# Optimization experiments

Hardware: AMD Instinct MI355X
Metric: run time of the kernel (lower is better)

The kernel has to match this reference:

```python
import jax, jax.numpy as jnp
from jax import lax
import numpy as np

B, T, D_IN, H, L, D_OUT = 1024, 512, 6, 128, 3, 1


def _lstm_layer(xs, w_ih, w_hh, b_ih, b_hh):
    """xs: [B, T, Din]; w_ih: [4H, Din]; w_hh: [4H, H]. PyTorch gate order i,f,g,o."""
    Bq = xs.shape[0]
    Hq = w_hh.shape[1]
    # Precompute the input projection for all timesteps (compute-dense part).
    x_proj = jnp.einsum('btd,gd->btg', xs, w_ih) + (b_ih + b_hh)  # [B, T, 4H]

    def step(carry, xp):
        h, c = carry
        gates = xp + h @ w_hh.T  # [B, 4H]
        i, f, g, o = jnp.split(gates, 4, axis=-1)
        i = jax.nn.sigmoid(i)
        f = jax.nn.sigmoid(f)
        g = jnp.tanh(g)
        o = jax.nn.sigmoid(o)
        c = f * c + i * g
        h = o * jnp.tanh(c)
        return (h, c), h

    h0 = jnp.zeros((Bq, Hq), xs.dtype)
    c0 = jnp.zeros((Bq, Hq), xs.dtype)
    (_, _), hs = lax.scan(step, (h0, c0), jnp.swapaxes(x_proj, 0, 1))  # hs: [T, B, H]
    return jnp.swapaxes(hs, 0, 1)  # [B, T, H]


def setup_inputs() -> dict:
    key = jax.random.key(0)
    ks = jax.random.split(key, 16)
    s = 1.0 / np.sqrt(H)  # PyTorch LSTM init scale
    inp = {"x": jax.random.normal(ks[0], (B, T, D_IN), dtype=jnp.float32)}
    din = D_IN
    for l in range(L):
        inp[f"w_ih{l}"] = jax.random.uniform(ks[1 + 4 * l], (4 * H, din), minval=-s, maxval=s, dtype=jnp.float32)
        inp[f"w_hh{l}"] = jax.random.uniform(ks[2 + 4 * l], (4 * H, H), minval=-s, maxval=s, dtype=jnp.float32)
        inp[f"b_ih{l}"] = jax.random.uniform(ks[3 + 4 * l], (4 * H,), minval=-s, maxval=s, dtype=jnp.float32)
        inp[f"b_hh{l}"] = jax.random.uniform(ks[4 + 4 * l], (4 * H,), minval=-s, maxval=s, dtype=jnp.float32)
        din = H
    inp["fc_w"] = jax.random.uniform(ks[13], (D_OUT, H), minval=-s, maxval=s, dtype=jnp.float32)
    inp["fc_b"] = jax.random.uniform(ks[14], (D_OUT,), minval=-s, maxval=s, dtype=jnp.float32)
    return inp


def reference(x, w_ih0, w_hh0, b_ih0, b_hh0, w_ih1, w_hh1, b_ih1, b_hh1,
              w_ih2, w_hh2, b_ih2, b_hh2, fc_w, fc_b):
    # 3-layer LSTM (inference: dropout between layers is identity) + final Linear on last timestep.
    h = _lstm_layer(x, w_ih0, w_hh0, b_ih0, b_hh0)
    h = _lstm_layer(h, w_ih1, w_hh1, b_ih1, b_hh1)
    h = _lstm_layer(h, w_ih2, w_hh2, b_ih2, b_hh2)
    return h[:, -1, :] @ fc_w.T + fc_b  # [B, 1]
```

## Files before the change

### kernel.cpp

```cpp
#include <hip/hip_runtime.h>

#define TLEN  512
#define HID   128
#define RSLOT 16
#define QD    4

typedef __attribute__((ext_vector_type(8))) short          bf16x8;
typedef __attribute__((ext_vector_type(4))) float          f32x4;
typedef __attribute__((ext_vector_type(4))) unsigned short u16x4;
typedef unsigned long long u64;

#define LOG2E  1.4426950408889634f
#define LOG2E2 2.8853900817779268f

__device__ __forceinline__ unsigned short f2bf(float f) {
    union { float f; unsigned u; } v; v.f = f;
    unsigned r = v.u + 0x7fffu + ((v.u >> 16) & 1u);
    return (unsigned short)(r >> 16);
}
__device__ __forceinline__ unsigned short f2bf_fast(float f) {
    union { float f; unsigned u; } v; v.f = f;
    return (unsigned short)((v.u + 0x8000u) >> 16);
}

__device__ __forceinline__ float sig_ps(float xs) {
    return __builtin_amdgcn_rcpf(1.0f + __builtin_exp2f(-xs));
}
__device__ __forceinline__ float tanh_ps(float xs) {
    return 2.0f * __builtin_amdgcn_rcpf(1.0f + __builtin_exp2f(-xs)) - 1.0f;
}

__device__ __forceinline__ int flag_peek(const int* f) {
    return __hip_atomic_load(f, __ATOMIC_RELAXED, __HIP_MEMORY_SCOPE_AGENT);
}
__device__ __forceinline__ int flag_spin(const int* f, int v) {
    int x = flag_peek(f);
    while (x < v) { __builtin_amdgcn_s_sleep(1); x = flag_peek(f); }
    return x;
}
__device__ __forceinline__ void flag_pub(int* f, int v) {
    __hip_atomic_store(f, v, __ATOMIC_RELAXED, __HIP_MEMORY_SCOPE_WORKGROUP);
}

template<int MODE, bool CONS, bool PROD, bool WFC>
__device__ __forceinline__ void run_layer_p(
    const float* __restrict__ xin,
    const u64* __restrict__ rin, u64* __restrict__ rout,
    const int* pin_flag, int* cout_flag, const int* cin_flag, int* pout_flag,
    const float* __restrict__ wih, const float* __restrict__ whh,
    const float* __restrict__ bih, const float* __restrict__ bhh,
    unsigned short (* __restrict__ Abuf)[8 * 512],
    float* __restrict__ fcred,
    const int tid, const int wave, const int lane,
    const int n16, const int quad, const int bbase)
{
    constexpr int NKT  = MODE ? 8 : 5;
    constexpr int KX   = MODE ? 128 : 32;
    constexpr int DINL = MODE ? 128 : 6;
    constexpr int HB0  = MODE ? 2048 : 512;

    bf16x8 Wf[4][NKT];
    float  bb[4];
#pragma unroll
    for (int g = 0; g < 4; ++g) {
        const float sc = (g == 2) ? LOG2E2 : LOG2E;
        const int row = g * 128 + wave * 16 + n16;
        bb[g] = (bih[row] + bhh[row]) * sc;
#pragma unroll
        for (int kt = 0; kt < NKT; ++kt) {
            const int kbase = kt * 32 + quad * 8;
            bf16x8 wv;
#pragma unroll
            for (int j = 0; j < 8; ++j) {
                const int k = kbase + j;
                float f;
                if (k < KX) f = (k < DINL) ? wih[row * DINL + k] : 0.0f;
                else        f = whh[row * HID + (k - KX)];
                wv[j] = (short)f2bf(f * sc);
            }
            Wf[g][kt] = wv;
        }
    }

    { u16x4 z = {0, 0, 0, 0}; *(u16x4*)&Abuf[0][HB0 + tid * 4] = z; }
    u64 q[QD - 1]; u64 qn = 0;
#pragma unroll
    for (int i = 0; i < QD - 1; ++i) q[i] = 0;
    float pfx0 = 0.0f;
    int pend = 0, cpend = 0;
    if constexpr (CONS) {
        flag_spin(pin_flag, 1);
        u64 v0 = __hip_atomic_load(rin + tid, __ATOMIC_RELAXED, __HIP_MEMORY_SCOPE_AGENT);
        *(u64*)&Abuf[0][tid * 4] = v0;
        pend = flag_spin(pin_flag, QD);
#pragma unroll
        for (int i = 0; i < QD - 1; ++i)
            q[i] = __hip_atomic_load(rin + (i + 1) * 512 + tid, __ATOMIC_RELAXED, __HIP_MEMORY_SCOPE_AGENT);
    } else {
        const int m = tid >> 5, k = tid & 31;
        float v = (k < DINL) ? xin[((bbase + m) * TLEN + 0) * DINL + k] : 0.0f;
        Abuf[0][((k >> 3) * 16 + m) * 8 + (k & 7)] = f2bf(v);
        if (k < DINL) pfx0 = xin[((bbase + m) * TLEN + 1) * DINL + k];
    }
    if constexpr (PROD) cpend = -(1 << 30);

    float cst[4] = {0.f, 0.f, 0.f, 0.f};

    for (int t = 0; t < TLEN; ++t) {
        const int cur = t & 1, nxt = cur ^ 1;
        __syncthreads();

        if constexpr (CONS) {
            if (t + QD < TLEN) {
                if (pend < t + QD + 1) pend = flag_spin(pin_flag, t + QD + 1);
                qn = __hip_atomic_load(rin + ((t + QD) & (RSLOT - 1)) * 512 + tid,
                                       __ATOMIC_RELAXED, __HIP_MEMORY_SCOPE_AGENT);
                pend = flag_peek(pin_flag);
            }
        }

        if (tid == 0) {
            if constexpr (CONS)
                if ((t & 3) == 0)
                    flag_pub(cout_flag, t + QD);
            if constexpr (PROD)
                if (t >= 2)
                    flag_pub(pout_flag, t - 1);
        }

        if constexpr (PROD) {
            if (t >= 1) {
                const int e = t - 1;
                if ((e & 3) == 0 && e + 4 > RSLOT && cpend < e + 4 - RSLOT)
                    cpend = flag_spin(cin_flag, e + 4 - RSLOT);
                u64 hv = *(const u64*)&Abuf[cur][HB0 + tid * 4];
                __hip_atomic_store(rout + (e & (RSLOT - 1)) * 512 + tid, hv,
                                   __ATOMIC_RELAXED, __HIP_MEMORY_SCOPE_WORKGROUP);
                if ((e & 3) == 1) cpend = flag_peek(cin_flag);
            }
        }

        float pfx1 = 0.0f;
        if constexpr (!CONS) {
            if (t + 2 < TLEN) {
                const int m = tid >> 5, k = tid & 31;
                if (k < DINL) pfx1 = xin[((bbase + m) * TLEN + (t + 2)) * DINL + k];
            }
        }

        f32x4 acc[4];
#pragma unroll
        for (int g = 0; g < 4; ++g) {
            f32x4 bi = {bb[g], bb[g], bb[g], bb[g]};
            acc[g] = bi;
        }
#pragma unroll
        for (int kt = 0; kt < NKT; ++kt) {
            bf16x8 a = *(const bf16x8*)&Abuf[cur][kt * 512 + lane * 8];
#pragma unroll
            for (int g = 0; g < 4; ++g)
                acc[g] = __builtin_amdgcn_mfma_f32_16x16x32_bf16(a, Wf[g][kt], acc[g], 0, 0, 0);
        }

        unsigned short hb[4]; float hf[4];
#pragma unroll
        for (int r = 0; r < 4; ++r) {
            const float iv = sig_ps (acc[0][r]);
            const float fv = sig_ps (acc[1][r]);
            const float gv = tanh_ps(acc[2][r]);
            const float ov = sig_ps (acc[3][r]);
            const float c  = fv * cst[r] + iv * gv;
            cst[r] = c;
            const float h  = ov * tanh_ps(c * LOG2E2);
            hf[r] = h;
            hb[r] = f2bf_fast(h);
        }

        {
            const int j  = wave * 16 + n16;
            const int kh = KX + j;
            const int kt = kh >> 5, kk = kh & 31;
            const int eb = kt * 512 + (kk >> 3) * 128 + (kk & 7);
#pragma unroll
            for (int r = 0; r < 4; ++r)
                Abuf[nxt][eb + (quad * 4 + r) * 8] = hb[r];
        }
        if constexpr (WFC) {
            if (t == TLEN - 1)
#pragma unroll
                for (int r = 0; r < 4; ++r)
                    fcred[(quad * 4 + r) * HID + wave * 16 + n16] = hf[r];
        }

        if (t + 1 < TLEN) {
            if constexpr (CONS) {
                *(u64*)&Abuf[nxt][tid * 4] = q[0];
#pragma unroll
                for (int i = 0; i < QD - 2; ++i) q[i] = q[i + 1];
                q[QD - 2] = qn;
            } else {
                const int m = tid >> 5, k = tid & 31;
                Abuf[nxt][((k >> 3) * 16 + m) * 8 + (k & 7)] = f2bf(pfx0);
                pfx0 = pfx1;
            }
        }
    }

    if constexpr (PROD) {
        __syncthreads();
        if (tid == 0)
            flag_pub(pout_flag, TLEN - 1);
        {
            flag_spin(cin_flag, TLEN - RSLOT);
            u64 hv = *(const u64*)&Abuf[TLEN & 1][HB0 + tid * 4];
            __hip_atomic_store(rout + ((TLEN - 1) & (RSLOT - 1)) * 512 + tid, hv,
                               __ATOMIC_RELAXED, __HIP_MEMORY_SCOPE_WORKGROUP);
        }
        __syncthreads();
        if (tid == 0)
            flag_pub(pout_flag, TLEN);
    }
}

extern "C" __global__ __launch_bounds__(512, 2)
void lstm3_pipe_kernel(const float* __restrict__ xin,
    const float* __restrict__ wih0, const float* __restrict__ whh0,
    const float* __restrict__ bih0, const float* __restrict__ bhh0,
    const float* __restrict__ wih1, const float* __restrict__ whh1,
    const float* __restrict__ bih1, const float* __restrict__ bhh1,
    const float* __restrict__ wih2, const float* __restrict__ whh2,
    const float* __restrict__ bih2, const float* __restrict__ bhh2,
    const float* __restrict__ fcw, const float* __restrict__ fcb,
    float* __restrict__ out,
    int* __restrict__ flags, u64* __restrict__ ring0, u64* __restrict__ ring1)
{
    __shared__ unsigned short Abuf[2][8 * 512];
    __shared__ float fcred[16 * HID];

    const int tid   = threadIdx.x;
    const int wave  = tid >> 6;
    const int lane  = tid & 63;
    const int n16   = lane & 15;
    const int quad  = lane >> 4;

    const int xcd    = blockIdx.x & 7;
    const int grp    = blockIdx.x >> 3;
    const int layer  = grp % 3;
    const int sgroup = grp / 3;
    const int slice  = sgroup * 8 + xcd;
    const int bbase  = slice * 16;

    u64* r0 = ring0 + (size_t)slice * (RSLOT * 512);
    u64* r1 = ring1 + (size_t)slice * (RSLOT * 512);
    int* prod0 = flags + (size_t)(0 * 64 + slice) * 64;
    int* prod1 = flags + (size_t)(1 * 64 + slice) * 64;
    int* cons1 = flags + (size_t)(2 * 64 + slice) * 64;
    int* cons2 = flags + (size_t)(3 * 64 + slice) * 64;

    if (layer == 0) {
        run_layer_p<0, false, true, false>(xin, nullptr, r0,
            nullptr, nullptr, cons1, prod0,
            wih0, whh0, bih0, bhh0, Abuf, fcred, tid, wave, lane, n16, quad, bbase);
    } else if (layer == 1) {
        run_layer_p<1, true, true, false>(nullptr, r0, r1,
            prod0, cons1, cons2, prod1,
            wih1, whh1, bih1, bhh1, Abuf, fcred, tid, wave, lane, n16, quad, bbase);
    } else {
        run_layer_p<1, true, false, true>(nullptr, r1, nullptr,
            prod1, cons2, nullptr, nullptr,
            wih2, whh2, bih2, bhh2, Abuf, fcred, tid, wave, lane, n16, quad, bbase);
        __syncthreads();
        if (tid < 16) {
            float s = 0.0f;
#pragma unroll 8
            for (int j = 0; j < HID; ++j) s += fcw[j] * fcred[tid * HID + j];
            out[bbase + tid] = s + fcb[0];
        }
    }
}

extern "C" void kernel_launch(void* const* d_in, const int* in_sizes, int n_in,
                              void* d_out, int out_size, void* d_ws, size_t ws_size,
                              hipStream_t stream) {
    (void)in_sizes; (void)n_in; (void)out_size; (void)ws_size;
    const float* x    = (const float*)d_in[0];
    const float* wih0 = (const float*)d_in[1];
    const float* whh0 = (const float*)d_in[2];
    const float* bih0 = (const float*)d_in[3];
    const float* bhh0 = (const float*)d_in[4];
    const float* wih1 = (const float*)d_in[5];
    const float* whh1 = (const float*)d_in[6];
    const float* bih1 = (const float*)d_in[7];
    const float* bhh1 = (const float*)d_in[8];
    const float* wih2 = (const float*)d_in[9];
    const float* whh2 = (const float*)d_in[10];
    const float* bih2 = (const float*)d_in[11];
    const float* bhh2 = (const float*)d_in[12];
    const float* fcw  = (const float*)d_in[13];
    const float* fcb  = (const float*)d_in[14];
    float* out = (float*)d_out;

    int* flags = (int*)d_ws;
    u64* ring0 = (u64*)((char*)d_ws + 65536);
    u64* ring1 = ring0 + (size_t)64 * RSLOT * 512;

    lstm3_pipe_kernel<<<dim3(192), dim3(512), 0, stream>>>(
        x, wih0, whh0, bih0, bhh0, wih1, whh1, bih1, bhh1,
        wih2, whh2, bih2, bhh2, fcw, fcb, out, flags, ring0, ring1);
}
```

Measured before the change: 838.0 us.

## Split x and h MFMAs and compute next-step input projection off the critical path

Separates the combined A buffer into an h buffer and a triple-buffered x buffer, so the input-projection MFMAs for step t+1 are issued during step t after the recurrent MFMAs. Only the h-dependent 4 k-tiles remain on the serial recurrence, shortening the per-step dependency chain. The producer/consumer ring lookahead deepens by one, and launch bounds drop to 1 block per SIMD group to allow more registers for the double accumulator set. The cost is more registers, more LDS, and changed occupancy hints.

```diff
diff --git a/kernel.cpp b/kernel.cpp
--- a/kernel.cpp
+++ b/kernel.cpp
@@ -3,7 +3,6 @@
 #define TLEN  512
 #define HID   128
 #define RSLOT 16
-#define QD    4
 
 typedef __attribute__((ext_vector_type(8))) short          bf16x8;
 typedef __attribute__((ext_vector_type(4))) float          f32x4;
@@ -49,17 +48,16 @@
     const int* pin_flag, int* cout_flag, const int* cin_flag, int* pout_flag,
     const float* __restrict__ wih, const float* __restrict__ whh,
     const float* __restrict__ bih, const float* __restrict__ bhh,
-    unsigned short (* __restrict__ Abuf)[8 * 512],
+    unsigned short (* __restrict__ hbuf)[2048],
+    unsigned short (* __restrict__ xbuf)[2048],
     float* __restrict__ fcred,
     const int tid, const int wave, const int lane,
     const int n16, const int quad, const int bbase)
 {
-    constexpr int NKT  = MODE ? 8 : 5;
-    constexpr int KX   = MODE ? 128 : 32;
+    constexpr int NKTX = MODE ? 4 : 1;
     constexpr int DINL = MODE ? 128 : 6;
-    constexpr int HB0  = MODE ? 2048 : 512;
-
-    bf16x8 Wf[4][NKT];
+
+    bf16x8 Wfx[4][NKTX], Wfh[4][4];
     float  bb[4];
 #pragma unroll
     for (int g = 0; g < 4; ++g) {
@@ -67,123 +65,140 @@
         const int row = g * 128 + wave * 16 + n16;
         bb[g] = (bih[row] + bhh[row]) * sc;
 #pragma unroll
-        for (int kt = 0; kt < NKT; ++kt) {
-            const int kbase = kt * 32 + quad * 8;
+        for (int kt = 0; kt < NKTX; ++kt) {
             bf16x8 wv;
 #pragma unroll
             for (int j = 0; j < 8; ++j) {
-                const int k = kbase + j;
-                float f;
-                if (k < KX) f = (k < DINL) ? wih[row * DINL + k] : 0.0f;
-                else        f = whh[row * HID + (k - KX)];
-                wv[j] = (short)f2bf(f * sc);
-            }
-            Wf[g][kt] = wv;
-        }
-    }
-
-    { u16x4 z = {0, 0, 0, 0}; *(u16x4*)&Abuf[0][HB0 + tid * 4] = z; }
-    u64 q[QD - 1]; u64 qn = 0;
-#pragma unroll
-    for (int i = 0; i < QD - 1; ++i) q[i] = 0;
+                const int k = kt * 32 + quad * 8 + j;
+                wv[j] = (short)f2bf(((k < DINL) ? wih[row * DINL + k] : 0.0f) * sc);
+            }
+            Wfx[g][kt] = wv;
+        }
+#pragma unroll
+        for (int kt = 0; kt < 4; ++kt) {
+            bf16x8 wv;
+#pragma unroll
+            for (int j = 0; j < 8; ++j) {
+                const int k = kt * 32 + quad * 8 + j;
+                wv[j] = (short)f2bf(whh[row * HID + k] * sc);
+            }
+            Wfh[g][kt] = wv;
+        }
+    }
+
+    { u16x4 z = {0, 0, 0, 0}; *(u16x4*)&hbuf[0][tid * 4] = z; }
+    u64 q0 = 0, q1 = 0, q2 = 0, qn = 0;
     float pfx0 = 0.0f;
     int pend = 0, cpend = 0;
+    const int xm = tid >> 5, xk = tid & 31;
     if constexpr (CONS) {
         flag_spin(pin_flag, 1);
-        u64 v0 = __hip_atomic_load(rin + tid, __ATOMIC_RELAXED, __HIP_MEMORY_SCOPE_AGENT);
-        *(u64*)&Abuf[0][tid * 4] = v0;
-        pend = flag_spin(pin_flag, QD);
-#pragma unroll
-        for (int i = 0; i < QD - 1; ++i)
-            q[i] = __hip_atomic_load(rin + (i + 1) * 512 + tid, __ATOMIC_RELAXED, __HIP_MEMORY_SCOPE_AGENT);
+        *(u64*)&xbuf[0][tid * 4] =
+            __hip_atomic_load(rin + tid, __ATOMIC_RELAXED, __HIP_MEMORY_SCOPE_AGENT);
+        flag_spin(pin_flag, 2);
+        *(u64*)&xbuf[1][tid * 4] =
+            __hip_atomic_load(rin + 512 + tid, __ATOMIC_RELAXED, __HIP_MEMORY_SCOPE_AGENT);
+        pend = flag_spin(pin_flag, 5);
+        q0 = __hip_atomic_load(rin + 2 * 512 + tid, __ATOMIC_RELAXED, __HIP_MEMORY_SCOPE_AGENT);
+        q1 = __hip_atomic_load(rin + 3 * 512 + tid, __ATOMIC_RELAXED, __HIP_MEMORY_SCOPE_AGENT);
+        q2 = __hip_atomic_load(rin + 4 * 512 + tid, __ATOMIC_RELAXED, __HIP_MEMORY_SCOPE_AGENT);
     } else {
-        const int m = tid >> 5, k = tid & 31;
-        float v = (k < DINL) ? xin[((bbase + m) * TLEN + 0) * DINL + k] : 0.0f;
-        Abuf[0][((k >> 3) * 16 + m) * 8 + (k & 7)] = f2bf(v);
-        if (k < DINL) pfx0 = xin[((bbase + m) * TLEN + 1) * DINL + k];
+        const int ei = ((xk >> 3) * 16 + xm) * 8 + (xk & 7);
+        float v0 = (xk < DINL) ? xin[((bbase + xm) * TLEN + 0) * DINL + xk] : 0.0f;
+        float v1 = (xk < DINL) ? xin[((bbase + xm) * TLEN + 1) * DINL + xk] : 0.0f;
+        xbuf[0][ei] = f2bf(v0);
+        xbuf[1][ei] = f2bf(v1);
+        if (xk < DINL) pfx0 = xin[((bbase + xm) * TLEN + 2) * DINL + xk];
     }
     if constexpr (PROD) cpend = -(1 << 30);
+    __syncthreads();
+
+    f32x4 accA[4], accB[4];
+#pragma unroll
+    for (int g = 0; g < 4; ++g) { f32x4 bi = {bb[g], bb[g], bb[g], bb[g]}; accA[g] = bi; }
+#pragma unroll
+    for (int kt = 0; kt < NKTX; ++kt) {
+        bf16x8 a = *(const bf16x8*)&xbuf[0][kt * 512 + lane * 8];
+#pragma unroll
+        for (int g = 0; g < 4; ++g)
+            accA[g] = __builtin_amdgcn_mfma_f32_16x16x32_bf16(a, Wfx[g][kt], accA[g], 0, 0, 0);
+    }
 
     float cst[4] = {0.f, 0.f, 0.f, 0.f};
-
-    for (int t = 0; t < TLEN; ++t) {
+    int rd = 1, wr = 2;
+
+    auto step = [&](f32x4 (&accC)[4], f32x4 (&accN)[4], int t) {
         const int cur = t & 1, nxt = cur ^ 1;
         __syncthreads();
 
         if constexpr (CONS) {
-            if (t + QD < TLEN) {
-                if (pend < t + QD + 1) pend = flag_spin(pin_flag, t + QD + 1);
-                qn = __hip_atomic_load(rin + ((t + QD) & (RSLOT - 1)) * 512 + tid,
+            if (t + 5 < TLEN) {
+                if (pend < t + 6) pend = flag_spin(pin_flag, t + 6);
+                qn = __hip_atomic_load(rin + ((t + 5) & (RSLOT - 1)) * 512 + tid,
                                        __ATOMIC_RELAXED, __HIP_MEMORY_SCOPE_AGENT);
                 pend = flag_peek(pin_flag);
             }
         }
-
         if (tid == 0) {
-            if constexpr (CONS)
-                if ((t & 3) == 0)
-                    flag_pub(cout_flag, t + QD);
-            if constexpr (PROD)
-                if (t >= 2)
-                    flag_pub(pout_flag, t - 1);
-        }
-
+            if constexpr (CONS) if ((t & 3) == 0) flag_pub(cout_flag, t + 5);
+            if constexpr (PROD) if (t >= 2)       flag_pub(pout_flag, t - 1);
+        }
         if constexpr (PROD) {
             if (t >= 1) {
                 const int e = t - 1;
                 if ((e & 3) == 0 && e + 4 > RSLOT && cpend < e + 4 - RSLOT)
                     cpend = flag_spin(cin_flag, e + 4 - RSLOT);
-                u64 hv = *(const u64*)&Abuf[cur][HB0 + tid * 4];
+                u64 hv = *(const u64*)&hbuf[cur][tid * 4];
                 __hip_atomic_store(rout + (e & (RSLOT - 1)) * 512 + tid, hv,
                                    __ATOMIC_RELAXED, __HIP_MEMORY_SCOPE_WORKGROUP);
                 if ((e & 3) == 1) cpend = flag_peek(cin_flag);
             }
         }
-
         float pfx1 = 0.0f;
         if constexpr (!CONS) {
-            if (t + 2 < TLEN) {
-                const int m = tid >> 5, k = tid & 31;
-                if (k < DINL) pfx1 = xin[((bbase + m) * TLEN + (t + 2)) * DINL + k];
-            }
-        }
-
-        f32x4 acc[4];
-#pragma unroll
-        for (int g = 0; g < 4; ++g) {
-            f32x4 bi = {bb[g], bb[g], bb[g], bb[g]};
-            acc[g] = bi;
-        }
-#pragma unroll
-        for (int kt = 0; kt < NKT; ++kt) {
-            bf16x8 a = *(const bf16x8*)&Abuf[cur][kt * 512 + lane * 8];
+            if (t + 3 < TLEN && xk < DINL)
+                pfx1 = xin[((bbase + xm) * TLEN + (t + 3)) * DINL + xk];
+        }
+
+#pragma unroll
+        for (int kt = 0; kt < 4; ++kt) {
+            bf16x8 a = *(const bf16x8*)&hbuf[cur][kt * 512 + lane * 8];
 #pragma unroll
             for (int g = 0; g < 4; ++g)
-                acc[g] = __builtin_amdgcn_mfma_f32_16x16x32_bf16(a, Wf[g][kt], acc[g], 0, 0, 0);
+                accC[g] = __builtin_amdgcn_mfma_f32_16x16x32_bf16(a, Wfh[g][kt], accC[g], 0, 0, 0);
+        }
+
+        if (t + 1 < TLEN) {
+#pragma unroll
+            for (int g = 0; g < 4; ++g) { f32x4 bi = {bb[g], bb[g], bb[g], bb[g]}; accN[g] = bi; }
+#pragma unroll
+            for (int kt = 0; kt < NKTX; ++kt) {
+                bf16x8 a = *(const bf16x8*)&xbuf[rd][kt * 512 + lane * 8];
+#pragma unroll
+                for (int g = 0; g < 4; ++g)
+                    accN[g] = __builtin_amdgcn_mfma_f32_16x16x32_bf16(a, Wfx[g][kt], accN[g], 0, 0, 0);
+            }
         }
 
         unsigned short hb[4]; float hf[4];
 #pragma unroll
         for (int r = 0; r < 4; ++r) {
-            const float iv = sig_ps (acc[0][r]);
-            const float fv = sig_ps (acc[1][r]);
-            const float gv = tanh_ps(acc[2][r]);
-            const float ov = sig_ps (acc[3][r]);
+            const float iv = sig_ps (accC[0][r]);
+            const float fv = sig_ps (accC[1][r]);
+            const float gv = tanh_ps(accC[2][r]);
+            const float ov = sig_ps (accC[3][r]);
             const float c  = fv * cst[r] + iv * gv;
             cst[r] = c;
             const float h  = ov * tanh_ps(c * LOG2E2);
             hf[r] = h;
             hb[r] = f2bf_fast(h);
         }
-
         {
             const int j  = wave * 16 + n16;
-            const int kh = KX + j;
-            const int kt = kh >> 5, kk = kh & 31;
-            const int eb = kt * 512 + (kk >> 3) * 128 + (kk & 7);
+            const int eb = (j >> 5) * 512 + (((j & 31) >> 3) * 16) * 8 + ((j & 31) & 7);
 #pragma unroll
             for (int r = 0; r < 4; ++r)
-                Abuf[nxt][eb + (quad * 4 + r) * 8] = hb[r];
+                hbuf[nxt][eb + (quad * 4 + r) * 8] = hb[r];
         }
         if constexpr (WFC) {
             if (t == TLEN - 1)
@@ -191,38 +206,38 @@
                 for (int r = 0; r < 4; ++r)
                     fcred[(quad * 4 + r) * HID + wave * 16 + n16] = hf[r];
         }
-
-        if (t + 1 < TLEN) {
+        if (t + 2 < TLEN) {
             if constexpr (CONS) {
-                *(u64*)&Abuf[nxt][tid * 4] = q[0];
-#pragma unroll
-                for (int i = 0; i < QD - 2; ++i) q[i] = q[i + 1];
-                q[QD - 2] = qn;
+                *(u64*)&xbuf[wr][tid * 4] = q0;
+                q0 = q1; q1 = q2; q2 = qn;
             } else {
-                const int m = tid >> 5, k = tid & 31;
-                Abuf[nxt][((k >> 3) * 16 + m) * 8 + (k & 7)] = f2bf(pfx0);
+                xbuf[wr][((xk >> 3) * 16 + xm) * 8 + (xk & 7)] = f2bf(pfx0);
                 pfx0 = pfx1;
             }
         }
+        rd = wr; wr = (wr == 2) ? 0 : wr + 1;
+    };
+
+    for (int t = 0; t < TLEN; t += 2) {
+        step(accA, accB, t);
+        step(accB, accA, t + 1);
     }
 
     if constexpr (PROD) {
         __syncthreads();
-        if (tid == 0)
-            flag_pub(pout_flag, TLEN - 1);
+        if (tid == 0) flag_pub(pout_flag, TLEN - 1);
         {
             flag_spin(cin_flag, TLEN - RSLOT);
-            u64 hv = *(const u64*)&Abuf[TLEN & 1][HB0 + tid * 4];
+            u64 hv = *(const u64*)&hbuf[TLEN & 1][tid * 4];
             __hip_atomic_store(rout + ((TLEN - 1) & (RSLOT - 1)) * 512 + tid, hv,
                                __ATOMIC_RELAXED, __HIP_MEMORY_SCOPE_WORKGROUP);
         }
         __syncthreads();
-        if (tid == 0)
-            flag_pub(pout_flag, TLEN);
-    }
-}
-
-extern "C" __global__ __launch_bounds__(512, 2)
+        if (tid == 0) flag_pub(pout_flag, TLEN);
+    }
+}
+
+extern "C" __global__ __launch_bounds__(512, 1)
 void lstm3_pipe_kernel(const float* __restrict__ xin,
     const float* __restrict__ wih0, const float* __restrict__ whh0,
     const float* __restrict__ bih0, const float* __restrict__ bhh0,
@@ -234,7 +249,8 @@
     float* __restrict__ out,
     int* __restrict__ flags, u64* __restrict__ ring0, u64* __restrict__ ring1)
 {
-    __shared__ unsigned short Abuf[2][8 * 512];
+    __shared__ unsigned short hbuf[2][2048];
+    __shared__ unsigned short xbuf[3][2048];
     __shared__ float fcred[16 * HID];
 
     const int tid   = threadIdx.x;
@@ -260,15 +276,15 @@
     if (layer == 0) {
         run_layer_p<0, false, true, false>(xin, nullptr, r0,
             nullptr, nullptr, cons1, prod0,
-            wih0, whh0, bih0, bhh0, Abuf, fcred, tid, wave, lane, n16, quad, bbase);
+            wih0, whh0, bih0, bhh0, hbuf, xbuf, fcred, tid, wave, lane, n16, quad, bbase);
     } else if (layer == 1) {
         run_layer_p<1, true, true, false>(nullptr, r0, r1,
             prod0, cons1, cons2, prod1,
-            wih1, whh1, bih1, bhh1, Abuf, fcred, tid, wave, lane, n16, quad, bbase);
+            wih1, whh1, bih1, bhh1, hbuf, xbuf, fcred, tid, wave, lane, n16, quad, bbase);
     } else {
         run_layer_p<1, true, false, true>(nullptr, r1, nullptr,
             prod1, cons2, nullptr, nullptr,
-            wih2, whh2, bih2, bhh2, Abuf, fcred, tid, wave, lane, n16, quad, bbase);
+            wih2, whh2, bih2, bhh2, hbuf, xbuf, fcred, tid, wave, lane, n16, quad, bbase);
         __syncthreads();
         if (tid < 16) {
             float s = 0.0f;
```

After: 833.6 us. Within noise of the previous version (-0.5%).
